# Performance work log

Measured on AMD Instinct MI355X. Metric: run time of the kernel, lower is better.

Reference implementation:

```python
import jax, jax.numpy as jnp
import numpy as np

PAD = 0
B, S, D, H, NH, PF, V, NMAX, L = 32, 512, 256, 512, 8, 2048, 100000, 15, 2
HD = H // NH


def setup_inputs() -> dict:
    key = jax.random.key(0)
    ks = iter(jax.random.split(key, 40))
    N = B * S
    p = lambda *s: jax.random.normal(next(ks), s, dtype=jnp.float32) * 0.02
    return dict(
        src=jax.random.randint(next(ks), (B, S), 0, V),
        src_lengths=jax.random.randint(next(ks), (B,), 1, S + 1),
        neighbor_idx=jax.random.randint(next(ks), (N, NMAX), 0, N),
        neighbor_count=jax.random.randint(next(ks), (N,), 0, NMAX + 1),
        time_intervals=jax.random.uniform(next(ks), (B, S), dtype=jnp.float32),
        emb=p(V, D).at[PAD].set(0.0),
        time_W=p(D), time_b=p(D),
        soc_W=p(D, D), soc_b=p(D), soc_g=jnp.ones(D), soc_beta=jnp.zeros(D),
        proj_W=p(D, H), proj_b=p(H),
        Wq=p(L, H, H), bq=p(L, H), Wk=p(L, H, H), bk=p(L, H),
        Wv=p(L, H, H), bv=p(L, H), Wo=p(L, H, H), bo=p(L, H),
        ln1_g=jnp.ones((L, H)), ln1_b=jnp.zeros((L, H)),
        ff_W1=p(L, H, PF), ff_b1=p(L, PF), ff_W2=p(L, PF, H), ff_b2=p(L, H),
        ln2_g=jnp.ones((L, H)), ln2_b=jnp.zeros((L, H)),
    )


def _ln(x, g, b):
    mu = x.mean(-1, keepdims=True)
    v = ((x - mu) ** 2).mean(-1, keepdims=True)
    return (x - mu) / jnp.sqrt(v + 1e-5) * g + b


def _forward(src, neighbor_idx, neighbor_count, time_intervals, emb, time_W, time_b,
             soc_W, soc_b, soc_g, soc_beta, proj_W, proj_b,
             Wq, bq, Wk, bk, Wv, bv, Wo, bo, ln1_g, ln1_b,
             ff_W1, ff_b1, ff_W2, ff_b2, ln2_g, ln2_b):
    # embedding + sinusoidal positional encoding
    x = emb[src]  # [B,S,D]
    pos = jnp.arange(S, dtype=jnp.float32)[:, None]
    div = jnp.exp(jnp.arange(0, D, 2, dtype=jnp.float32) * (-np.log(10000.0) / D))
    pe = jnp.zeros((S, D)).at[:, 0::2].set(jnp.sin(pos * div)).at[:, 1::2].set(jnp.cos(pos * div))
    x = x + pe
    # time interval encoding: Linear(1, D) on t[...,None]
    x = x + time_intervals[..., None] * time_W + time_b
    # neighbor aggregation (batched form of the per-node loop: mean over <=15 valid neighbors)
    N = B * S
    flat = x.reshape(N, D)
    nb = flat[neighbor_idx]  # [N, NMAX, D] irregular gather
    m = (jnp.arange(NMAX)[None, :] < neighbor_count[:, None]).astype(flat.dtype)
    agg = (nb * m[..., None]).sum(1) / jnp.maximum(neighbor_count, 1).astype(flat.dtype)[:, None]
    soc = jax.nn.relu(_ln(flat + agg @ soc_W + soc_b, soc_g, soc_beta))
    soc = jnp.where((neighbor_count > 0)[:, None], soc, flat)  # no neighbors -> passthrough
    soc = jnp.where((src.reshape(N) != PAD)[:, None], soc, 0.0)  # only valid (non-PAD) tokens
    x = x + 0.2 * soc.reshape(B, S, D)
    # transformer encoder stack
    h = x @ proj_W + proj_b
    kmask = src != PAD  # [B,S]
    for l in range(L):
        q = (h @ Wq[l] + bq[l]).reshape(B, S, NH, HD)
        k = (h @ Wk[l] + bk[l]).reshape(B, S, NH, HD)
        v = (h @ Wv[l] + bv[l]).reshape(B, S, NH, HD)
        e = jnp.einsum('bqhd,bkhd->bhqk', q, k) / jnp.sqrt(jnp.float32(HD))
        e = jnp.where(kmask[:, None, None, :], e, -1e10)
        a = jax.nn.softmax(e, axis=-1)
        o = jnp.einsum('bhqk,bkhd->bqhd', a, v).reshape(B, S, H)
        h = _ln(h + o @ Wo[l] + bo[l], ln1_g[l], ln1_b[l])
        ff = jax.nn.relu(h @ ff_W1[l] + ff_b1[l]) @ ff_W2[l] + ff_b2[l]
        h = _ln(h + ff, ln2_g[l], ln2_b[l])
    return h, x  # (src_out, embedded)


def reference(src, src_lengths, neighbor_idx, neighbor_count, time_intervals, emb, time_W, time_b,
              soc_W, soc_b, soc_g, soc_beta, proj_W, proj_b,
              Wq, bq, Wk, bk, Wv, bv, Wo, bo, ln1_g, ln1_b,
              ff_W1, ff_b1, ff_W2, ff_b2, ln2_g, ln2_b):
    # src_lengths unused by the original forward
    return _forward(src, neighbor_idx, neighbor_count, time_intervals, emb, time_W, time_b,
                    soc_W, soc_b, soc_g, soc_beta, proj_W, proj_b,
                    Wq, bq, Wk, bk, Wv, bv, Wo, bo, ln1_g, ln1_b,
                    ff_W1, ff_b1, ff_W2, ff_b2, ln2_g, ln2_b)
```

## Files before the change

kernel.cpp:

```cpp
#include <hip/hip_runtime.h>

#define BB 32
#define SS 512
#define DD 256
#define HHH 512
#define NHH 8
#define HDD 64
#define PFF 2048
#define LLL 2
#define NN (BB*SS)
#define NMAXX 15

typedef unsigned short u16;
typedef unsigned int u32;

typedef __attribute__((ext_vector_type(8))) __bf16 bf16x8;
typedef __attribute__((ext_vector_type(4))) float f32x4;

__device__ __forceinline__ float bf2f(u16 u) {
  union { u32 i; float f; } x; x.i = ((u32)u) << 16; return x.f;
}
__device__ __forceinline__ u16 f2bf(float f) {
  union { float f; u32 i; } x; x.f = f;
  u32 r = x.i + 0x7FFFu + ((x.i >> 16) & 1u);
  return (u16)(r >> 16);
}
__device__ __forceinline__ float ldf(const void* p, size_t i, int flag) {
  return flag ? bf2f(((const u16*)p)[i]) : ((const float*)p)[i];
}
__device__ __forceinline__ void stf(void* p, size_t i, int flag, float v) {
  if (flag) ((u16*)p)[i] = f2bf(v); else ((float*)p)[i] = v;
}
__device__ __forceinline__ void gld16(const u16* g, u16* l) {
  __builtin_amdgcn_global_load_lds(
      (const __attribute__((address_space(1))) u32*)g,
      (__attribute__((address_space(3))) u32*)l, 16, 0, 0);
}

__global__ void k_flag(const u32* __restrict__ ones, int* __restrict__ flag) {
  *flag = (ones[0] == 0x3F800000u) ? 0 : 1;
}

__global__ __launch_bounds__(256) void k_transpose_f(const void* __restrict__ in, size_t ioff,
    u16* __restrict__ out, int R, int C, const int* __restrict__ flagp) {
  __shared__ u16 tile[32][33];
  int flag = *flagp;
  int c0 = blockIdx.x * 32, r0 = blockIdx.y * 32;
  int tx = threadIdx.x, ty = threadIdx.y;
  #pragma unroll
  for (int i = 0; i < 4; ++i)
    tile[ty + i*8][tx] = f2bf(ldf(in, ioff + (size_t)(r0 + ty + i*8) * C + c0 + tx, flag));
  __syncthreads();
  #pragma unroll
  for (int i = 0; i < 4; ++i) out[(size_t)(c0 + ty + i*8) * R + r0 + tx] = tile[tx][ty + i*8];
}

__global__ __launch_bounds__(256) void k_packb(const void* __restrict__ projb,
    const void* __restrict__ bq, const void* __restrict__ bk, const void* __restrict__ bv,
    const void* __restrict__ b1, const void* __restrict__ bo, const void* __restrict__ b2,
    u16* __restrict__ out, const int* __restrict__ flagp) {
  int flag = *flagp;
  int i = blockIdx.x * 256 + threadIdx.x;
  int tot = 512 + LLL * 4608;
  if (i >= tot) return;
  float v;
  if (i < 512) v = ldf(projb, i, flag);
  else {
    int j = i - 512, l = j / 4608, r = j % 4608;
    if      (r < 512)  v = ldf(bq, (size_t)l * HHH + r, flag);
    else if (r < 1024) v = ldf(bk, (size_t)l * HHH + r - 512, flag);
    else if (r < 1536) v = ldf(bv, (size_t)l * HHH + r - 1024, flag);
    else if (r < 3584) v = ldf(b1, (size_t)l * PFF + r - 1536, flag);
    else if (r < 4096) v = ldf(bo, (size_t)l * HHH + r - 3584, flag);
    else               v = ldf(b2, (size_t)l * HHH + r - 4096, flag);
  }
  out[i] = f2bf(v);
}

__global__ __launch_bounds__(256) void k_embed(const int* __restrict__ src,
    const void* __restrict__ tiv, const void* __restrict__ emb,
    const void* __restrict__ tW, const void* __restrict__ tB,
    u16* __restrict__ X, const int* __restrict__ flagp) {
  int flag = *flagp;
  int n = blockIdx.x, d = threadIdx.x;
  int s = n & (SS - 1);
  int tok = src[n];
  float v = ldf(emb, (size_t)tok * DD + d, flag);
  int i2 = d & ~1;
  float freq = expf(-0.035977892078031968f * (float)i2);
  float ang = (float)s * freq;
  v += (d & 1) ? cosf(ang) : sinf(ang);
  float t = ldf(tiv, n, flag);
  v += t * ldf(tW, d, flag) + ldf(tB, d, flag);
  X[(size_t)n * DD + d] = f2bf(v);
}

__global__ __launch_bounds__(256) void k_agg(const int* __restrict__ nidx,
    const int* __restrict__ ncnt, const u16* __restrict__ X, u16* __restrict__ AGG) {
  int n = blockIdx.x, d = threadIdx.x;
  int cnt = ncnt[n];
  float s = 0.f;
  for (int j = 0; j < cnt; ++j) {
    int m = nidx[n * NMAXX + j];
    s += bf2f(X[(size_t)m * DD + d]);
  }
  float div = (float)(cnt > 0 ? cnt : 1);
  AGG[(size_t)n * DD + d] = f2bf(s / div);
}

__global__ __launch_bounds__(256) void k_gemm128(const u16* __restrict__ A,
    const u16* __restrict__ BT, const void* __restrict__ bias, int boff,
    const u16* __restrict__ res, u16* __restrict__ C, int N, int K, int relu,
    const int* __restrict__ flagp) {
  __shared__ __align__(16) u16 As[128 * 32];
  __shared__ __align__(16) u16 Bs[128 * 32];
  int n0 = blockIdx.x * 128, m0 = blockIdx.y * 128;
  int t = threadIdx.x;
  int lane = t & 63, w = t >> 6;
  int wm = (w >> 1) * 64, wn = (w & 1) * 64;
  int fr = lane & 15, fq = lane >> 4;
  int srow = t >> 2, sseg = t & 3;

  f32x4 acc[4][4];
  #pragma unroll
  for (int i = 0; i < 4; ++i)
    #pragma unroll
    for (int j = 0; j < 4; ++j) acc[i][j] = (f32x4){0.f, 0.f, 0.f, 0.f};

  const u16* ga = A  + (size_t)(m0 + srow) * K + sseg * 8;
  const u16* gb = BT + (size_t)(n0 + srow) * K + sseg * 8;
  u16* lA = As + srow * 32 + sseg * 8;
  u16* lB = Bs + srow * 32 + sseg * 8;
  const size_t rstride = (size_t)64 * K;

  for (int k0 = 0; k0 < K; k0 += 32) {
    gld16(ga + k0, lA);
    gld16(ga + k0 + rstride, lA + 64 * 32);
    gld16(gb + k0, lB);
    gld16(gb + k0 + rstride, lB + 64 * 32);
    __syncthreads();
    bf16x8 af[4], bf[4];
    #pragma unroll
    for (int i = 0; i < 4; ++i) af[i] = *(const bf16x8*)&As[(wm + i * 16 + fr) * 32 + fq * 8];
    #pragma unroll
    for (int j = 0; j < 4; ++j) bf[j] = *(const bf16x8*)&Bs[(wn + j * 16 + fr) * 32 + fq * 8];
    #pragma unroll
    for (int i = 0; i < 4; ++i)
      #pragma unroll
      for (int j = 0; j < 4; ++j)
        acc[i][j] = __builtin_amdgcn_mfma_f32_16x16x32_bf16(af[i], bf[j], acc[i][j], 0, 0, 0);
    __syncthreads();
  }

  int flag = *flagp;
  #pragma unroll
  for (int j = 0; j < 4; ++j) {
    int col = n0 + wn + j * 16 + fr;
    float bv = bias ? ldf(bias, boff + col, flag) : 0.f;
    #pragma unroll
    for (int i = 0; i < 4; ++i) {
      #pragma unroll
      for (int c = 0; c < 4; ++c) {
        int row = m0 + wm + i * 16 + fq * 4 + c;
        float v = acc[i][j][c] + bv;
        if (res) v += bf2f(res[(size_t)row * N + col]);
        if (relu) v = fmaxf(v, 0.f);
        C[(size_t)row * N + col] = f2bf(v);
      }
    }
  }
}

template<int NBF>
__global__ __launch_bounds__(512, 2) void k_gemm256(const u16* __restrict__ A,
    const u16* __restrict__ BT, const u16* __restrict__ bias,
    u16* __restrict__ C, int N, int K, int relu, int nbx) {
  constexpr int AG = 1024;
  constexpr int BG = NBF * 256;
  constexpr int STRIDE = (AG + BG) * 8;
  constexpr int LPT = 2 + BG / 512;
  __shared__ __align__(16) u16 S[3 * STRIDE];

  int nwg = gridDim.x;
  int id = blockIdx.x;
  int wg = ((nwg & 7) == 0) ? ((id & 7) * (nwg >> 3) + (id >> 3)) : id;
  int bx = wg % nbx, by = wg / nbx;
  int m0 = by * 256, n0 = bx * (64 * NBF);

  int t = threadIdx.x;
  int w = t >> 6, lane = t & 63;
  int fr = lane & 15, fq = lane >> 4;
  int wm = (w >> 2) * 128, wn = (w & 3) * (16 * NBF);
  int gsw8 = (fq ^ (fr & 3) ^ ((fr >> 2) & 3)) * 8;

  int arow = t >> 2, aseg = t & 3;
  int asw = aseg ^ (arow & 3) ^ ((arow >> 2) & 3);
  const u16* gA  = A  + (size_t)(m0 + arow) * K + asw * 8;
  const u16* gA2 = gA + (size_t)128 * K;
  const u16* gB  = BT + (size_t)(n0 + arow) * K + asw * 8;
  const u16* gB2 = gB + (size_t)128 * K;

  f32x4 acc[8][NBF];
  #pragma unroll
  for (int i = 0; i < 8; ++i)
    #pragma unroll
    for (int j = 0; j < NBF; ++j) acc[i][j] = (f32x4){0.f, 0.f, 0.f, 0.f};

  int NT = K >> 5;

  #pragma unroll
  for (int p = 0; p < 2; ++p) {
    gld16(gA  + p * 32, S + p * STRIDE + t * 8);
    gld16(gA2 + p * 32, S + p * STRIDE + (t + 512) * 8);
    gld16(gB  + p * 32, S + p * STRIDE + AG * 8 + t * 8);
    if constexpr (NBF == 4)
      gld16(gB2 + p * 32, S + p * STRIDE + AG * 8 + (t + 512) * 8);
  }
  asm volatile("s_waitcnt vmcnt(%0)" :: "n"(LPT) : "memory");
  __builtin_amdgcn_s_barrier();
  __builtin_amdgcn_sched_barrier(0);

  for (int T = 0; T < NT; ++T) {
    const u16* Sa = S + (T % 3) * STRIDE;
    const u16* Sb = Sa + AG * 8;
    u16* Sn = S + ((T + 2) % 3) * STRIDE;
    int kn = (T + 2) * 32;
    bool st = (T + 2) < NT;

    bf16x8 af[4], bf[NBF];
    #pragma unroll
    for (int i = 0; i < 4; ++i) af[i] = *(const bf16x8*)&Sa[(wm + i * 16 + fr) * 32 + gsw8];
    #pragma unroll
    for (int j = 0; j < NBF; ++j) bf[j] = *(const bf16x8*)&Sb[(wn + j * 16 + fr) * 32 + gsw8];
    if (st) {
      gld16(gA  + kn, Sn + t * 8);
      gld16(gA2 + kn, Sn + (t + 512) * 8);
    }
    __builtin_amdgcn_s_setprio(1);
    #pragma unroll
    for (int i = 0; i < 4; ++i)
      #pragma unroll
      for (int j = 0; j < NBF; ++j)
        acc[i][j] = __builtin_amdgcn_mfma_f32_16x16x32_bf16(af[i], bf[j], acc[i][j], 0, 0, 0);
    __builtin_amdgcn_s_setprio(0);

    bf16x8 ag[4];
    #pragma unroll
    for (int i = 0; i < 4; ++i) ag[i] = *(const bf16x8*)&Sa[(wm + 64 + i * 16 + fr) * 32 + gsw8];
    if (st) {
      gld16(gB + kn, Sn + AG * 8 + t * 8);
      if constexpr (NBF == 4)
        gld16(gB2 + kn, Sn + AG * 8 + (t + 512) * 8);
    }
    __builtin_amdgcn_s_setprio(1);
    #pragma unroll
    for (int i = 0; i < 4; ++i)
      #pragma unroll
      for (int j = 0; j < NBF; ++j)
        acc[4 + i][j] = __builtin_amdgcn_mfma_f32_16x16x32_bf16(ag[i], bf[j], acc[4 + i][j], 0, 0, 0);
    __builtin_amdgcn_s_setprio(0);

    if (st) { asm volatile("s_waitcnt vmcnt(%0) lgkmcnt(0)" :: "n"(LPT) : "memory"); }
    else    { asm volatile("s_waitcnt vmcnt(0) lgkmcnt(0)" ::: "memory"); }
    __builtin_amdgcn_s_barrier();
    __builtin_amdgcn_sched_barrier(0);
  }

  #pragma unroll
  for (int j = 0; j < NBF; ++j) {
    int col = n0 + wn + j * 16 + fr;
    float bv = bf2f(bias[col]);
    #pragma unroll
    for (int i = 0; i < 8; ++i) {
      #pragma unroll
      for (int c = 0; c < 4; ++c) {
        int row = m0 + wm + i * 16 + fq * 4 + c;
        float v = acc[i][j][c] + bv;
        if (relu) v = fmaxf(v, 0.f);
        C[(size_t)row * N + col] = f2bf(v);
      }
    }
  }
}

__global__ __launch_bounds__(256) void k_ln_soc(const u16* __restrict__ socp,
    const u16* __restrict__ X, const void* __restrict__ g, const void* __restrict__ beta,
    const int* __restrict__ ncnt, const int* __restrict__ src,
    u16* __restrict__ X2, void* __restrict__ dout, const int* __restrict__ flagp) {
  __shared__ float sred[4];
  int flag = *flagp;
  int n = blockIdx.x, t = threadIdx.x;
  size_t base = (size_t)n * DD;
  float v = bf2f(socp[base + t]);
  float s = v;
  #pragma unroll
  for (int o = 32; o; o >>= 1) s += __shfl_xor(s, o, 64);
  if ((t & 63) == 0) sred[t >> 6] = s;
  __syncthreads();
  float mean = (sred[0] + sred[1] + sred[2] + sred[3]) * (1.f / DD);
  float dv = v - mean;
  float q = dv * dv;
  #pragma unroll
  for (int o = 32; o; o >>= 1) q += __shfl_xor(q, o, 64);
  __syncthreads();
  if ((t & 63) == 0) sred[t >> 6] = q;
  __syncthreads();
  float var = (sred[0] + sred[1] + sred[2] + sred[3]) * (1.f / DD);
  float rs = rsqrtf(var + 1e-5f);
  float soc = fmaxf(dv * rs * ldf(g, t, flag) + ldf(beta, t, flag), 0.f);
  float xv = bf2f(X[base + t]);
  if (ncnt[n] <= 0) soc = xv;
  if (src[n] == 0)  soc = 0.f;
  float ov = xv + 0.2f * soc;
  X2[base + t] = f2bf(ov);
  stf(dout, (size_t)NN * HHH + base + t, flag, ov);
}

__global__ __launch_bounds__(256) void k_ln_add(const u16* __restrict__ a,
    const u16* __restrict__ b, const void* __restrict__ g, int goff,
    const void* __restrict__ bb, int boff, u16* __restrict__ out,
    const int* __restrict__ flagp) {
  __shared__ float sred[4];
  int flag = *flagp;
  int row = blockIdx.x, t = threadIdx.x;
  size_t base = (size_t)row * HHH;
  float v0 = bf2f(a[base + t])       + bf2f(b[base + t]);
  float v1 = bf2f(a[base + 256 + t]) + bf2f(b[base + 256 + t]);
  float s = v0 + v1;
  #pragma unroll
  for (int o = 32; o; o >>= 1) s += __shfl_xor(s, o, 64);
  if ((t & 63) == 0) sred[t >> 6] = s;
  __syncthreads();
  float mean = (sred[0] + sred[1] + sred[2] + sred[3]) * (1.f / HHH);
  float d0 = v0 - mean, d1 = v1 - mean;
  float q = d0 * d0 + d1 * d1;
  #pragma unroll
  for (int o = 32; o; o >>= 1) q += __shfl_xor(q, o, 64);
  __syncthreads();
  if ((t & 63) == 0) sred[t >> 6] = q;
  __syncthreads();
  float var = (sred[0] + sred[1] + sred[2] + sred[3]) * (1.f / HHH);
  float rs = rsqrtf(var + 1e-5f);
  out[base + t]       = f2bf(d0 * rs * ldf(g, goff + t, flag)       + ldf(bb, boff + t, flag));
  out[base + 256 + t] = f2bf(d1 * rs * ldf(g, goff + 256 + t, flag) + ldf(bb, boff + 256 + t, flag));
}

__global__ __launch_bounds__(512, 2) void k_attn_mfma(const u16* __restrict__ Q,
    const u16* __restrict__ Kb, const u16* __restrict__ Vb, int ld,
    const int* __restrict__ src, u16* __restrict__ O) {
  __shared__ __align__(16) u16 Ks[512 * 64];
  __shared__ __align__(16) u16 VTs[64 * 512];
  __shared__ __align__(16) u16 Ps[128 * 72];
  __shared__ float maskv[512];
  int h = blockIdx.x, b = blockIdx.y;
  int t = threadIdx.x;
  int w = t >> 6, lane = t & 63;
  int fr = lane & 15, fq = lane >> 4;

  maskv[t] = (src[b * SS + t] != 0) ? 1.f : 0.f;

  #pragma unroll
  for (int i = 0; i < 8; ++i) {
    int off = t + i * 512;
    int row = off >> 3;
    int gs  = (off & 7) ^ (row & 7);
    gld16(Kb + (size_t)(b * SS + row) * ld + h * HDD + gs * 8, Ks + (size_t)off * 8);
  }
  {
    const u16* vsrc = Vb + (size_t)(b * SS + t) * ld + h * HDD;
    int ghi = (t >> 3) & ~7, glo = (t >> 3) & 7, kw = t & 7;
    #pragma unroll
    for (int i = 0; i < 8; ++i) {
      uint4 raw = *(const uint4*)(vsrc + i * 8);
      u16 e[8]; *(uint4*)e = raw;
      #pragma unroll
      for (int jj = 0; jj < 8; ++jj) {
        int d = i * 8 + jj;
        VTs[(size_t)d * 512 + (size_t)((ghi | (glo ^ (d & 7))) * 8 + kw)] = e[jj];
      }
    }
  }
  __syncthreads();

  for (int chunk = 0; chunk < 4; ++chunk) {
    int qb = chunk * 128 + w * 16;
    bf16x8 qf[2];
    #pragma unroll
    for (int kc = 0; kc < 2; ++kc)
      qf[kc] = *(const bf16x8*)&Q[(size_t)(b * SS + qb + fr) * ld + h * HDD + kc * 32 + fq * 8];

    f32x4 sacc[32];
    #pragma unroll
    for (int j = 0; j < 32; ++j) sacc[j] = (f32x4){0.f, 0.f, 0.f, 0.f};

    #pragma unroll
    for (int kt = 0; kt < 32; ++kt) {
      int row = kt * 16 + fr;
      #pragma unroll
      for (int kc = 0; kc < 2; ++kc) {
        bf16x8 kf = *(const bf16x8*)&Ks[(size_t)row * 64 +
            (size_t)(((kc * 4 + fq) ^ (fr & 7)) * 8)];
        sacc[kt] = __builtin_amdgcn_mfma_f32_16x16x32_bf16(qf[kc], kf, sacc[kt], 0, 0, 0);
      }
    }

    #pragma unroll
    for (int j = 0; j < 32; ++j) {
      float mv = maskv[j * 16 + fr];
      #pragma unroll
      for (int c = 0; c < 4; ++c) {
        float v = sacc[j][c] * 0.125f;
        sacc[j][c] = (mv != 0.f) ? v : -1e10f;
      }
    }
    #pragma unroll
    for (int c = 0; c < 4; ++c) {
      float m = -3.0e38f;
      #pragma unroll
      for (int j = 0; j < 32; ++j) m = fmaxf(m, sacc[j][c]);
      #pragma unroll
      for (int o = 1; o < 16; o <<= 1) m = fmaxf(m, __shfl_xor(m, o, 64));
      float s = 0.f;
      #pragma unroll
      for (int j = 0; j < 32; ++j) { float e = __expf(sacc[j][c] - m); sacc[j][c] = e; s += e; }
      #pragma unroll
      for (int o = 1; o < 16; o <<= 1) s += __shfl_xor(s, o, 64);
      float inv = 1.f / s;
      #pragma unroll
      for (int j = 0; j < 32; ++j) sacc[j][c] *= inv;
    }

    f32x4 oacc[4];
    #pragma unroll
    for (int n = 0; n < 4; ++n) oacc[n] = (f32x4){0.f, 0.f, 0.f, 0.f};

    #pragma unroll
    for (int seg = 0; seg < 8; ++seg) {
      #pragma unroll
      for (int tt = 0; tt < 4; ++tt)
        #pragma unroll
        for (int c = 0; c < 4; ++c)
          Ps[(size_t)(w * 16 + fq * 4 + c) * 72 + tt * 16 + fr] = f2bf(sacc[seg * 4 + tt][c]);
      #pragma unroll
      for (int kc = 0; kc < 2; ++kc) {
        bf16x8 pa = *(const bf16x8*)&Ps[(size_t)(w * 16 + fr) * 72 + kc * 32 + fq * 8];
        #pragma unroll
        for (int nt = 0; nt < 4; ++nt) {
          bf16x8 bv = *(const bf16x8*)&VTs[(size_t)(nt * 16 + fr) * 512 +
              (size_t)((seg * 8 + ((kc * 4 + fq) ^ (fr & 7))) * 8)];
          oacc[nt] = __builtin_amdgcn_mfma_f32_16x16x32_bf16(pa, bv, oacc[nt], 0, 0, 0);
        }
      }
    }

    #pragma unroll
    for (int nt = 0; nt < 4; ++nt)
      #pragma unroll
      for (int c = 0; c < 4; ++c)
        O[(size_t)(b * SS + qb + fq * 4 + c) * HHH + h * HDD + nt * 16 + fr] = f2bf(oacc[nt][c]);
  }
}

__global__ __launch_bounds__(256) void k_out(const u16* __restrict__ Hb,
    void* __restrict__ out, const int* __restrict__ flagp) {
  int flag = *flagp;
  size_t i = ((size_t)blockIdx.x * 256 + threadIdx.x) * 4;
  if (flag) {
    *(uint2*)((u16*)out + i) = *(const uint2*)(Hb + i);
  } else {
    float4 v;
    v.x = bf2f(Hb[i]); v.y = bf2f(Hb[i+1]); v.z = bf2f(Hb[i+2]); v.w = bf2f(Hb[i+3]);
    *(float4*)((float*)out + i) = v;
  }
}

extern "C" void kernel_launch(void* const* d_in, const int* in_sizes, int n_in,
                              void* d_out, int out_size, void* d_ws, size_t ws_size,
                              hipStream_t stream) {
  (void)in_sizes; (void)n_in; (void)out_size; (void)ws_size;
  const int* src    = (const int*)d_in[0];
  const int* nidx   = (const int*)d_in[2];
  const int* ncnt   = (const int*)d_in[3];
  const void* tiv   = d_in[4];
  const void* emb   = d_in[5];
  const void* tW    = d_in[6];
  const void* tB    = d_in[7];
  const void* socW  = d_in[8];
  const void* socb  = d_in[9];
  const void* socg  = d_in[10];
  const void* socbe = d_in[11];
  const void* projW = d_in[12];
  const void* projb = d_in[13];
  const void* Wq    = d_in[14];
  const void* bq    = d_in[15];
  const void* Wk    = d_in[16];
  const void* bk    = d_in[17];
  const void* Wv    = d_in[18];
  const void* bv    = d_in[19];
  const void* Wo    = d_in[20];
  const void* bo    = d_in[21];
  const void* ln1g  = d_in[22];
  const void* ln1b  = d_in[23];
  const void* W1    = d_in[24];
  const void* b1    = d_in[25];
  const void* W2    = d_in[26];
  const void* b2    = d_in[27];
  const void* ln2g  = d_in[28];
  const void* ln2b  = d_in[29];

  const size_t NHS = (size_t)NN * HHH;
  const size_t QKV3 = (size_t)3 * HHH * HHH;
  u16* ws = (u16*)d_ws;
  u16* socWT  = ws;
  u16* projWT = socWT + (size_t)DD * DD;
  u16* WqkvT  = projWT + (size_t)DD * HHH;
  u16* WoT    = WqkvT + (size_t)LLL * QKV3;
  u16* W1T    = WoT + (size_t)LLL * HHH * HHH;
  u16* W2T    = W1T + (size_t)LLL * HHH * PFF;
  u16* Hb     = W2T + (size_t)LLL * HHH * PFF;
  u16* P1     = Hb + NHS;
  u16* P2     = P1 + NHS;
  u16* P3     = P2 + NHS;
  int* flagp  = (int*)(P3 + NHS);
  u16* packb  = (u16*)(flagp + 4);
  u16* X    = P1;
  u16* AGG  = P2;
  u16* SOCP = P3;
  u16* X2   = P2;
  u16* Ob   = (u16*)d_out;
  u16* FFM  = P2;

  k_flag<<<1, 1, 0, stream>>>((const u32*)ln1g, flagp);

  dim3 tb(32, 8);
  k_transpose_f<<<dim3(DD / 32, DD / 32), tb, 0, stream>>>(socW, 0, socWT, DD, DD, flagp);
  k_transpose_f<<<dim3(HHH / 32, DD / 32), tb, 0, stream>>>(projW, 0, projWT, DD, HHH, flagp);
  for (int l = 0; l < LLL; ++l) {
    size_t oHH = (size_t)l * HHH * HHH, oHP = (size_t)l * HHH * PFF;
    u16* wq = WqkvT + (size_t)l * QKV3;
    k_transpose_f<<<dim3(HHH / 32, HHH / 32), tb, 0, stream>>>(Wq, oHH, wq, HHH, HHH, flagp);
    k_transpose_f<<<dim3(HHH / 32, HHH / 32), tb, 0, stream>>>(Wk, oHH, wq + (size_t)HHH * HHH, HHH, HHH, flagp);
    k_transpose_f<<<dim3(HHH / 32, HHH / 32), tb, 0, stream>>>(Wv, oHH, wq + (size_t)2 * HHH * HHH, HHH, HHH, flagp);
    k_transpose_f<<<dim3(HHH / 32, HHH / 32), tb, 0, stream>>>(Wo, oHH, WoT + oHH, HHH, HHH, flagp);
    k_transpose_f<<<dim3(PFF / 32, HHH / 32), tb, 0, stream>>>(W1, oHP, W1T + oHP, HHH, PFF, flagp);
    k_transpose_f<<<dim3(HHH / 32, PFF / 32), tb, 0, stream>>>(W2, oHP, W2T + oHP, PFF, HHH, flagp);
  }
  k_packb<<<dim3((512 + LLL * 4608 + 255) / 256), 256, 0, stream>>>(
      projb, bq, bk, bv, b1, bo, b2, packb, flagp);

  k_embed<<<NN, 256, 0, stream>>>(src, tiv, emb, tW, tB, X, flagp);
  k_agg<<<NN, 256, 0, stream>>>(nidx, ncnt, X, AGG);
  k_gemm128<<<dim3(DD / 128, NN / 128), 256, 0, stream>>>(AGG, socWT, socb, 0, X, SOCP, DD, DD, 0, flagp);
  k_ln_soc<<<NN, 256, 0, stream>>>(SOCP, X, socg, socbe, ncnt, src, X2, d_out, flagp);
  k_gemm256<2><<<dim3(256), 512, 0, stream>>>(X2, projWT, packb, Hb, HHH, DD, 0, 4);

  for (int l = 0; l < LLL; ++l) {
    size_t oHH = (size_t)l * HHH * HHH, oHP = (size_t)l * HHH * PFF;
    u16* lb = packb + 512 + (size_t)l * 4608;
    k_gemm256<4><<<dim3(384), 512, 0, stream>>>(Hb, WqkvT + (size_t)l * QKV3, lb, P1, 1536, HHH, 0, 6);
    k_attn_mfma<<<dim3(NHH, BB), 512, 0, stream>>>(P1, P1 + HHH, P1 + 2 * HHH, 3 * HHH, src, Ob);
    k_gemm256<2><<<dim3(256), 512, 0, stream>>>(Ob, WoT + oHH, lb + 3584, P1, HHH, HHH, 0, 4);
    k_ln_add<<<NN, 256, 0, stream>>>(Hb, P1, ln1g, l * HHH, ln1b, l * HHH, Hb, flagp);
    for (int c = 0; c < 2; ++c) {
      const u16* Asrc = Hb + (size_t)c * 8192 * HHH;
      u16* Cdst = P1 + (size_t)c * 8192 * HHH;
      k_gemm256<4><<<dim3(256), 512, 0, stream>>>(Asrc, W1T + oHP, lb + 1536, FFM, PFF, HHH, 1, 8);
      k_gemm256<2><<<dim3(128), 512, 0, stream>>>(FFM, W2T + oHP, lb + 4096, Cdst, HHH, PFF, 0, 4);
    }
    k_ln_add<<<NN, 256, 0, stream>>>(Hb, P1, ln2g, l * HHH, ln2b, l * HHH, Hb, flagp);
  }
  k_out<<<dim3((unsigned)(NHS / 4 / 256)), 256, 0, stream>>>(Hb, d_out, flagp);
}
```

Before: 900.7 us.

## Precompute PE table, fuse output write into LN, unchunk FFN, vectorize attention store

Adds a small kernel that precomputes the sinusoidal positional encoding plus time bias once per position, so the embed kernel no longer evaluates exp/sin/cos per token. The final layer's LN writes straight to the output buffer, which removes the separate copy kernel. When the workspace is large enough, the FFN runs as one full-size GEMM pair instead of two chunks, cutting launches and tail effects. The attention output MFMA operands are swapped so each lane can store four contiguous bf16 values in one packed write instead of scattered 16-bit stores.

```diff
diff --git a/kernel.cpp b/kernel.cpp
--- a/kernel.cpp
+++ b/kernel.cpp
@@ -77,21 +77,29 @@
   out[i] = f2bf(v);
 }
 
+__global__ __launch_bounds__(256) void k_pe(const void* __restrict__ tB,
+    u16* __restrict__ pet, const int* __restrict__ flagp) {
+  int flag = *flagp;
+  int s = blockIdx.x, d = threadIdx.x;
+  int i2 = d & ~1;
+  float freq = expf(-0.035977892078031968f * (float)i2);
+  float ang = (float)s * freq;
+  float v = ((d & 1) ? cosf(ang) : sinf(ang)) + ldf(tB, d, flag);
+  pet[(size_t)s * DD + d] = f2bf(v);
+}
+
 __global__ __launch_bounds__(256) void k_embed(const int* __restrict__ src,
     const void* __restrict__ tiv, const void* __restrict__ emb,
-    const void* __restrict__ tW, const void* __restrict__ tB,
+    const void* __restrict__ tW, const u16* __restrict__ pet,
     u16* __restrict__ X, const int* __restrict__ flagp) {
   int flag = *flagp;
   int n = blockIdx.x, d = threadIdx.x;
   int s = n & (SS - 1);
   int tok = src[n];
   float v = ldf(emb, (size_t)tok * DD + d, flag);
-  int i2 = d & ~1;
-  float freq = expf(-0.035977892078031968f * (float)i2);
-  float ang = (float)s * freq;
-  v += (d & 1) ? cosf(ang) : sinf(ang);
+  v += bf2f(pet[(size_t)s * DD + d]);
   float t = ldf(tiv, n, flag);
-  v += t * ldf(tW, d, flag) + ldf(tB, d, flag);
+  v += t * ldf(tW, d, flag);
   X[(size_t)n * DD + d] = f2bf(v);
 }
 
@@ -319,7 +327,7 @@
 __global__ __launch_bounds__(256) void k_ln_add(const u16* __restrict__ a,
     const u16* __restrict__ b, const void* __restrict__ g, int goff,
     const void* __restrict__ bb, int boff, u16* __restrict__ out,
-    const int* __restrict__ flagp) {
+    void* __restrict__ dout, const int* __restrict__ flagp) {
   __shared__ float sred[4];
   int flag = *flagp;
   int row = blockIdx.x, t = threadIdx.x;
@@ -341,8 +349,15 @@
   __syncthreads();
   float var = (sred[0] + sred[1] + sred[2] + sred[3]) * (1.f / HHH);
   float rs = rsqrtf(var + 1e-5f);
-  out[base + t]       = f2bf(d0 * rs * ldf(g, goff + t, flag)       + ldf(bb, boff + t, flag));
-  out[base + 256 + t] = f2bf(d1 * rs * ldf(g, goff + 256 + t, flag) + ldf(bb, boff + 256 + t, flag));
+  float o0 = d0 * rs * ldf(g, goff + t, flag)       + ldf(bb, boff + t, flag);
+  float o1 = d1 * rs * ldf(g, goff + 256 + t, flag) + ldf(bb, boff + 256 + t, flag);
+  if (dout) {
+    stf(dout, base + t, flag, o0);
+    stf(dout, base + 256 + t, flag, o1);
+  } else {
+    out[base + t]       = f2bf(o0);
+    out[base + 256 + t] = f2bf(o1);
+  }
 }
 
 __global__ __launch_bounds__(512, 2) void k_attn_mfma(const u16* __restrict__ Q,
@@ -448,36 +463,25 @@
         for (int nt = 0; nt < 4; ++nt) {
           bf16x8 bv = *(const bf16x8*)&VTs[(size_t)(nt * 16 + fr) * 512 +
               (size_t)((seg * 8 + ((kc * 4 + fq) ^ (fr & 7))) * 8)];
-          oacc[nt] = __builtin_amdgcn_mfma_f32_16x16x32_bf16(pa, bv, oacc[nt], 0, 0, 0);
+          oacc[nt] = __builtin_amdgcn_mfma_f32_16x16x32_bf16(bv, pa, oacc[nt], 0, 0, 0);
         }
       }
     }
 
     #pragma unroll
-    for (int nt = 0; nt < 4; ++nt)
-      #pragma unroll
-      for (int c = 0; c < 4; ++c)
-        O[(size_t)(b * SS + qb + fq * 4 + c) * HHH + h * HDD + nt * 16 + fr] = f2bf(oacc[nt][c]);
-  }
-}
-
-__global__ __launch_bounds__(256) void k_out(const u16* __restrict__ Hb,
-    void* __restrict__ out, const int* __restrict__ flagp) {
-  int flag = *flagp;
-  size_t i = ((size_t)blockIdx.x * 256 + threadIdx.x) * 4;
-  if (flag) {
-    *(uint2*)((u16*)out + i) = *(const uint2*)(Hb + i);
-  } else {
-    float4 v;
-    v.x = bf2f(Hb[i]); v.y = bf2f(Hb[i+1]); v.z = bf2f(Hb[i+2]); v.w = bf2f(Hb[i+3]);
-    *(float4*)((float*)out + i) = v;
+    for (int nt = 0; nt < 4; ++nt) {
+      union { u16 e[4]; uint2 v; } pk;
+      #pragma unroll
+      for (int c = 0; c < 4; ++c) pk.e[c] = f2bf(oacc[nt][c]);
+      *(uint2*)&O[(size_t)(b * SS + qb + fr) * HHH + h * HDD + nt * 16 + fq * 4] = pk.v;
+    }
   }
 }
 
 extern "C" void kernel_launch(void* const* d_in, const int* in_sizes, int n_in,
                               void* d_out, int out_size, void* d_ws, size_t ws_size,
                               hipStream_t stream) {
-  (void)in_sizes; (void)n_in; (void)out_size; (void)ws_size;
+  (void)in_sizes; (void)n_in; (void)out_size;
   const int* src    = (const int*)d_in[0];
   const int* nidx   = (const int*)d_in[2];
   const int* ncnt   = (const int*)d_in[3];
@@ -523,12 +527,17 @@
   u16* P3     = P2 + NHS;
   int* flagp  = (int*)(P3 + NHS);
   u16* packb  = (u16*)(flagp + 4);
+  u16* pet    = packb + 16384;
+  u16* FFMf   = pet + (size_t)SS * DD;
+  size_t need_full = (size_t)(FFMf - ws + (size_t)NN * PFF) * 2;
+  int fullff = (ws_size >= need_full);
+
   u16* X    = P1;
   u16* AGG  = P2;
   u16* SOCP = P3;
   u16* X2   = P2;
   u16* Ob   = (u16*)d_out;
-  u16* FFM  = P2;
+  u16* FFMc = P2;
 
   k_flag<<<1, 1, 0, stream>>>((const u32*)ln1g, flagp);
 
@@ -547,8 +556,9 @@
   }
   k_packb<<<dim3((512 + LLL * 4608 + 255) / 256), 256, 0, stream>>>(
       projb, bq, bk, bv, b1, bo, b2, packb, flagp);
-
-  k_embed<<<NN, 256, 0, stream>>>(src, tiv, emb, tW, tB, X, flagp);
+  k_pe<<<SS, 256, 0, stream>>>(tB, pet, flagp);
+
+  k_embed<<<NN, 256, 0, stream>>>(src, tiv, emb, tW, pet, X, flagp);
   k_agg<<<NN, 256, 0, stream>>>(nidx, ncnt, X, AGG);
   k_gemm128<<<dim3(DD / 128, NN / 128), 256, 0, stream>>>(AGG, socWT, socb, 0, X, SOCP, DD, DD, 0, flagp);
   k_ln_soc<<<NN, 256, 0, stream>>>(SOCP, X, socg, socbe, ncnt, src, X2, d_out, flagp);
@@ -560,14 +570,19 @@
     k_gemm256<4><<<dim3(384), 512, 0, stream>>>(Hb, WqkvT + (size_t)l * QKV3, lb, P1, 1536, HHH, 0, 6);
     k_attn_mfma<<<dim3(NHH, BB), 512, 0, stream>>>(P1, P1 + HHH, P1 + 2 * HHH, 3 * HHH, src, Ob);
     k_gemm256<2><<<dim3(256), 512, 0, stream>>>(Ob, WoT + oHH, lb + 3584, P1, HHH, HHH, 0, 4);
-    k_ln_add<<<NN, 256, 0, stream>>>(Hb, P1, ln1g, l * HHH, ln1b, l * HHH, Hb, flagp);
-    for (int c = 0; c < 2; ++c) {
-      const u16* Asrc = Hb + (size_t)c * 8192 * HHH;
-      u16* Cdst = P1 + (size_t)c * 8192 * HHH;
-      k_gemm256<4><<<dim3(256), 512, 0, stream>>>(Asrc, W1T + oHP, lb + 1536, FFM, PFF, HHH, 1, 8);
-      k_gemm256<2><<<dim3(128), 512, 0, stream>>>(FFM, W2T + oHP, lb + 4096, Cdst, HHH, PFF, 0, 4);
-    }
-    k_ln_add<<<NN, 256, 0, stream>>>(Hb, P1, ln2g, l * HHH, ln2b, l * HHH, Hb, flagp);
-  }
-  k_out<<<dim3((unsigned)(NHS / 4 / 256)), 256, 0, stream>>>(Hb, d_out, flagp);
-}
+    k_ln_add<<<NN, 256, 0, stream>>>(Hb, P1, ln1g, l * HHH, ln1b, l * HHH, Hb, nullptr, flagp);
+    if (fullff) {
+      k_gemm256<4><<<dim3(512), 512, 0, stream>>>(Hb, W1T + oHP, lb + 1536, FFMf, PFF, HHH, 1, 8);
+      k_gemm256<2><<<dim3(256), 512, 0, stream>>>(FFMf, W2T + oHP, lb + 4096, P1, HHH, PFF, 0, 4);
+    } else {
+      for (int c = 0; c < 2; ++c) {
+        const u16* Asrc = Hb + (size_t)c * 8192 * HHH;
+        u16* Cdst = P1 + (size_t)c * 8192 * HHH;
+        k_gemm256<4><<<dim3(256), 512, 0, stream>>>(Asrc, W1T + oHP, lb + 1536, FFMc, PFF, HHH, 1, 8);
+        k_gemm256<2><<<dim3(128), 512, 0, stream>>>(FFMc, W2T + oHP, lb + 4096, Cdst, HHH, PFF, 0, 4);
+      }
+    }
+    void* dd = (l == LLL - 1) ? d_out : nullptr;
+    k_ln_add<<<NN, 256, 0, stream>>>(Hb, P1, ln2g, l * HHH, ln2b, l * HHH, Hb, dd, flagp);
+  }
+}
```

Measured after the change: 860.7 us. -4.4%, faster.
